# Kernel tuning notes

Measured on AMD Instinct MI355X. Metric: run time of the kernel, lower is better.

Reference implementation:

```python
import jax, jax.numpy as jnp
import numpy as np

B, H, W, C, D = 8, 64, 64, 128, 16


def setup_inputs() -> dict:
    key = jax.random.key(0)
    ks = jax.random.split(key, 6)
    scale = 1.0 / np.sqrt(C)
    return {
        "x": jax.random.normal(ks[0], (B, H, W, C), dtype=jnp.float32),
        "w_f": jax.random.normal(ks[1], (C, D), dtype=jnp.float32) * scale,
        "w_g": jax.random.normal(ks[2], (C, D), dtype=jnp.float32) * scale,
        "w_h": jax.random.normal(ks[3], (C, D), dtype=jnp.float32) * scale,
        "w_v": jax.random.normal(ks[4], (D, C), dtype=jnp.float32) * (1.0 / np.sqrt(D)),
        "gamma": jax.random.normal(ks[5], (1,), dtype=jnp.float32) * 0.1,
    }


def reference(x, w_f, w_g, w_h, w_v, gamma):
    b, h, w, c = x.shape
    n = h * w
    xf = x.reshape(b, n, c)                      # flatten spatial dims
    f = jnp.einsum('bnc,cd->bnd', xf, w_f)       # 1x1 conv == channel matmul
    g = jnp.einsum('bnc,cd->bnd', xf, w_g)
    hh = jnp.einsum('bnc,cd->bnd', xf, w_h)
    scores = jnp.einsum('bnd,bmd->bnm', f, g)    # [B, N, N], no 1/sqrt(d) scaling (faithful)
    attn = jax.nn.softmax(scores, axis=1)        # NOTE: softmax over axis=1 as in original
    y = jnp.einsum('bnm,bmd->bnd', attn, hh)     # [B, N, D]
    y = jnp.einsum('bnd,dc->bnc', y, w_v)        # output 1x1 conv
    y = y.reshape(b, h, w, c)
    return gamma * y + x
```

## Files before the change

### kernel.cpp

```cpp
#include <hip/hip_runtime.h>

typedef _Float16 f16;
typedef _Float16 f16x4 __attribute__((ext_vector_type(4)));
typedef _Float16 n16x2 __attribute__((ext_vector_type(2)));
typedef float    f32x4 __attribute__((ext_vector_type(4)));

#define LOG2E 1.44269504088896340736f
#define OFF25 36.0673760222824936f

__device__ __forceinline__ f32x4 MFMA(f16x4 a, f16x4 b, f32x4 c) {
#if defined(__HIP_DEVICE_COMPILE__)
    return __builtin_amdgcn_mfma_f32_16x16x16f16(a, b, c, 0, 0, 0);
#else
    return c;
#endif
}

__device__ __forceinline__ float fexp2(float x) {
#if defined(__HIP_DEVICE_COMPILE__)
    return __builtin_amdgcn_exp2f(x);
#else
    return exp2f(x);
#endif
}

__device__ __forceinline__ f16x4 pk4(float a, float b, float c, float d) {
#if defined(__HIP_DEVICE_COMPILE__)
    n16x2 lo = __builtin_bit_cast(n16x2, __builtin_amdgcn_cvt_pkrtz(a, b));
    n16x2 hi = __builtin_bit_cast(n16x2, __builtin_amdgcn_cvt_pkrtz(c, d));
    f16x4 r; r[0] = lo[0]; r[1] = lo[1]; r[2] = hi[0]; r[3] = hi[1];
    return r;
#else
    f16x4 r; r[0] = (f16)a; r[1] = (f16)b; r[2] = (f16)c; r[3] = (f16)d;
    return r;
#endif
}

__global__ __launch_bounds__(256) void k_proj(const float* __restrict__ x,
        const float* __restrict__ wf, const float* __restrict__ wg,
        const float* __restrict__ wh, f16* __restrict__ F,
        f16* __restrict__ G, float* __restrict__ Ht) {
    const int lane = threadIdx.x & 63;
    const int wid  = threadIdx.x >> 6;
    const int tile = wid >> 1;
    const int kh   = wid & 1;
    const int g16  = lane >> 4;
    const int c16  = lane & 15;
    const long r0  = ((long)blockIdx.x * 2 + tile) * 16;

    f16x4 bw[3][4];
    const float* Ws[3] = { wf, wg, wh };
    #pragma unroll
    for (int w = 0; w < 3; ++w)
        #pragma unroll
        for (int kk = 0; kk < 4; ++kk) {
            const int kb = (kh * 4 + kk) * 16 + g16 * 4;
            bw[w][kk] = pk4(Ws[w][(kb + 0) * 16 + c16], Ws[w][(kb + 1) * 16 + c16],
                            Ws[w][(kb + 2) * 16 + c16], Ws[w][(kb + 3) * 16 + c16]);
        }

    f32x4 af = {0,0,0,0}, ag = {0,0,0,0}, ah = {0,0,0,0};
    const float* xr = x + (r0 + c16) * 128;
    #pragma unroll
    for (int kk = 0; kk < 4; ++kk) {
        float4 xa = *(const float4*)(xr + (kh * 4 + kk) * 16 + g16 * 4);
        f16x4 a = pk4(xa.x, xa.y, xa.z, xa.w);
        af = MFMA(a, bw[0][kk], af);
        ag = MFMA(a, bw[1][kk], ag);
        ah = MFMA(a, bw[2][kk], ah);
    }

    __shared__ float red[2][64][13];
    if (kh == 1) {
        #pragma unroll
        for (int i = 0; i < 4; ++i) {
            red[tile][lane][i]     = af[i];
            red[tile][lane][4 + i] = ag[i];
            red[tile][lane][8 + i] = ah[i];
        }
    }
    __syncthreads();
    if (kh == 0) {
        #pragma unroll
        for (int i = 0; i < 4; ++i) {
            af[i] += red[tile][lane][i];
            ag[i] += red[tile][lane][4 + i];
            ah[i] += red[tile][lane][8 + i];
        }
        #pragma unroll
        for (int i = 0; i < 4; ++i) {
            const long row = r0 + g16 * 4 + i;
            F[row * 16 + c16] = (f16)(af[i] * LOG2E);
            G[row * 16 + c16] = (f16)ag[i];
        }
        float4 hv = make_float4(ah[0], ah[1], ah[2], ah[3]);
        *(float4*)(Ht + (long)c16 * 32768 + r0 + g16 * 4) = hv;
    }
}

__global__ __launch_bounds__(512) void k_cs(const f16* __restrict__ F,
        const f16* __restrict__ G, const float* __restrict__ Ht,
        float* __restrict__ nM2, f16* __restrict__ Hf) {
    const int lane = threadIdx.x & 63;
    const int tp   = threadIdx.x >> 6;
    const int b    = blockIdx.x >> 6;
    const int mb   = (blockIdx.x & 63) * 64;
    const int g16  = lane >> 4, c16 = lane & 15;
    const long bb  = (long)b * 4096;

    f16x4 ga[4];
    #pragma unroll
    for (int j = 0; j < 4; ++j)
        ga[j] = *(const f16x4*)(G + (bb + mb + 16 * j + c16) * 16 + g16 * 4);

    const f16* Fb = F + (bb + tp * 512) * 16;
    float qm[4][4], zs[4][4];
    #pragma unroll
    for (int j = 0; j < 4; ++j)
        #pragma unroll
        for (int i = 0; i < 4; ++i) { qm[j][i] = -1e30f; zs[j][i] = 0.f; }

    const f32x4 coff = {-OFF25, -OFF25, -OFF25, -OFF25};
    f16x4 fb0 = *(const f16x4*)(Fb + (c16) * 16 + g16 * 4);
    f16x4 fb1 = *(const f16x4*)(Fb + (16 + c16) * 16 + g16 * 4);
    f16x4 fb2 = *(const f16x4*)(Fb + (32 + c16) * 16 + g16 * 4);
    for (int t = 0; t < 32; ++t) {
        f16x4 fbn = *(const f16x4*)(Fb + ((t + 3) * 16 + c16) * 16 + g16 * 4);
        #pragma unroll
        for (int j = 0; j < 4; ++j) {
            f32x4 s = MFMA(ga[j], fb0, coff);
            #pragma unroll
            for (int i = 0; i < 4; ++i) {
                zs[j][i] += fexp2(s[i]);
                qm[j][i] = fmaxf(qm[j][i], s[i]);
            }
        }
        fb0 = fb1; fb1 = fb2; fb2 = fbn;
    }
    #pragma unroll
    for (int d = 8; d >= 1; d >>= 1)
        #pragma unroll
        for (int j = 0; j < 4; ++j)
            #pragma unroll
            for (int i = 0; i < 4; ++i) {
                qm[j][i] = fmaxf(qm[j][i], __shfl_xor(qm[j][i], d));
                zs[j][i] += __shfl_xor(zs[j][i], d);
            }

    __shared__ float lq[8][64], lz[8][64], lrz[64];
    if (c16 == 0) {
        #pragma unroll
        for (int j = 0; j < 4; ++j)
            #pragma unroll
            for (int i = 0; i < 4; ++i) {
                const int ml = 16 * j + 4 * g16 + i;
                lq[tp][ml] = qm[j][i];
                lz[tp][ml] = zs[j][i];
            }
    }
    __syncthreads();
    if (threadIdx.x < 64) {
        const int ml = threadIdx.x;
        float q = lq[0][ml], z = 0.f;
        #pragma unroll
        for (int p = 1; p < 8; ++p) q = fmaxf(q, lq[p][ml]);
        #pragma unroll
        for (int p = 0; p < 8; ++p) z += lz[p][ml];
        nM2[bb + mb + ml] = -q - OFF25;
        lrz[ml] = fexp2(q) / z;
    }
    __syncthreads();
    if (tp < 4) {
        const int ml0 = 16 * tp + 4 * g16;
        float4 hv = *(const float4*)(Ht + (long)c16 * 32768 + bb + mb + ml0);
        f32x4 rz = *(const f32x4*)&lrz[ml0];
        const long tileg = (bb + mb) / 16 + tp;
        *(f16x4*)(Hf + tileg * 256 + lane * 4) =
            pk4(hv.x * rz[0], hv.y * rz[1], hv.z * rz[2], hv.w * rz[3]);
    }
}

__global__ __launch_bounds__(512) void k_pv(const f16* __restrict__ F,
        const f16* __restrict__ G, const f16* __restrict__ Hf,
        const float* __restrict__ nM2, const float* __restrict__ wv,
        const float* __restrict__ xin, const float* __restrict__ gamma,
        float* __restrict__ out) {
    const int lane = threadIdx.x & 63;
    const int tp   = threadIdx.x >> 6;
    const int b    = blockIdx.x >> 6;
    const int n0   = (blockIdx.x & 63) * 64;
    const int g16  = lane >> 4, c16 = lane & 15;
    const long bb  = (long)b * 4096;

    f16x4 fbv[4];
    #pragma unroll
    for (int j = 0; j < 4; ++j)
        fbv[j] = *(const f16x4*)(F + (bb + n0 + 16 * j + c16) * 16 + g16 * 4);

    const int jo = tp >> 1, th = tp & 1;
    const float gm = gamma[0];
    f16x4 wvf[4];
    #pragma unroll
    for (int t = 0; t < 4; ++t) {
        const int c0 = (4 * th + t) * 16;
        wvf[t] = pk4(wv[(g16 * 4 + 0) * 128 + c0 + c16] * gm,
                     wv[(g16 * 4 + 1) * 128 + c0 + c16] * gm,
                     wv[(g16 * 4 + 2) * 128 + c0 + c16] * gm,
                     wv[(g16 * 4 + 3) * 128 + c0 + c16] * gm);
    }

    const f16* Gp = G + bb * 16;
    const f16* Hp = Hf + bb * 16 + lane * 4;
    const float* Np = nM2 + bb;
    const int mbase = tp * 512;

    f32x4 yT[4] = {{0,0,0,0},{0,0,0,0},{0,0,0,0},{0,0,0,0}};
    f16x4 ga0 = *(const f16x4*)(Gp + (mbase + c16) * 16 + g16 * 4);
    f16x4 ha0 = *(const f16x4*)(Hp + (long)mbase * 16);
    f32x4 nm0 = *(const f32x4*)(Np + mbase + g16 * 4);
    f16x4 ga1 = *(const f16x4*)(Gp + (mbase + 16 + c16) * 16 + g16 * 4);
    f16x4 ha1 = *(const f16x4*)(Hp + (long)(mbase + 16) * 16);
    f32x4 nm1 = *(const f32x4*)(Np + mbase + 16 + g16 * 4);
    f16x4 ga2 = *(const f16x4*)(Gp + (mbase + 32 + c16) * 16 + g16 * 4);
    f16x4 ha2 = *(const f16x4*)(Hp + (long)(mbase + 32) * 16);
    f32x4 nm2 = *(const f32x4*)(Np + mbase + 32 + g16 * 4);
    for (int t = 0; t < 32; ++t) {
        const int m3 = mbase + t * 16 + 48;
        f16x4 gan = *(const f16x4*)(Gp + (m3 + c16) * 16 + g16 * 4);
        f16x4 han = *(const f16x4*)(Hp + (long)m3 * 16);
        f32x4 nmn = *(const f32x4*)(Np + m3 + g16 * 4);
        #pragma unroll
        for (int j = 0; j < 4; ++j) {
            f32x4 s = MFMA(ga0, fbv[j], nm0);
            f16x4 pb = pk4(fexp2(s[0]), fexp2(s[1]),
                           fexp2(s[2]), fexp2(s[3]));
            yT[j] = MFMA(ha0, pb, yT[j]);
        }
        ga0 = ga1; ha0 = ha1; nm0 = nm1;
        ga1 = ga2; ha1 = ha2; nm1 = nm2;
        ga2 = gan; ha2 = han; nm2 = nmn;
    }

    __shared__ float red[8][4][64][5];
    #pragma unroll
    for (int j = 0; j < 4; ++j)
        #pragma unroll
        for (int i = 0; i < 4; ++i) red[tp][j][lane][i] = yT[j][i];
    __syncthreads();

    f32x4 ys = {0,0,0,0};
    #pragma unroll
    for (int p = 0; p < 8; ++p)
        #pragma unroll
        for (int i = 0; i < 4; ++i) ys[i] += red[p][jo][lane][i];
    const f16x4 ya = pk4(ys[0], ys[1], ys[2], ys[3]);

    #pragma unroll
    for (int t = 0; t < 4; ++t) {
        const int c0 = (4 * th + t) * 16;
        f32x4 zero = {0,0,0,0};
        f32x4 o = MFMA(ya, wvf[t], zero);
        #pragma unroll
        for (int i = 0; i < 4; ++i) {
            const long idx = (bb + n0 + 16 * jo + 4 * g16 + i) * 128 + c0 + c16;
            out[idx] = o[i] + xin[idx];
        }
    }
}

extern "C" void kernel_launch(void* const* d_in, const int* in_sizes, int n_in,
                              void* d_out, int out_size, void* d_ws, size_t ws_size,
                              hipStream_t stream) {
    const float* x     = (const float*)d_in[0];
    const float* wf    = (const float*)d_in[1];
    const float* wg    = (const float*)d_in[2];
    const float* wh    = (const float*)d_in[3];
    const float* wv    = (const float*)d_in[4];
    const float* gamma = (const float*)d_in[5];
    float* out = (float*)d_out;

    char* p = (char*)d_ws;
    const long BN  = 8L * 4096;
    const long PAD = 8192;
    f16*   F   = (f16*)p;    p += BN * 16 * sizeof(f16)   + PAD;
    f16*   G   = (f16*)p;    p += BN * 16 * sizeof(f16)   + PAD;
    float* Ht  = (float*)p;  p += 16 * BN * sizeof(float) + PAD;
    f16*   Hf  = (f16*)p;    p += 16 * BN * sizeof(f16)   + PAD;
    float* nM2 = (float*)p;  p += BN * sizeof(float)      + PAD;

    k_proj<<<1024, 256, 0, stream>>>(x, wf, wg, wh, F, G, Ht);
    k_cs  <<<512,  512, 0, stream>>>(F, G, Ht, nM2, Hf);
    k_pv  <<<512,  512, 0, stream>>>(F, G, Hf, nM2, wv, x, gamma, out);
}
```

Measured before the change: 54.44 us.

## Split attention reductions across two blocks with separate finalize and output kernels

Both the column-stats kernel and the PV kernel now split the reduction dimension in half across two blocks, doubling grid size from 512 to 1024 blocks so more CUs stay busy. Partial max/sum and partial Y results go to workspace, and two new kernels combine them: k_fin merges the stats and builds the scaled H, and k_out merges the Y halves and applies the Wv projection plus the gamma residual with scalar FMAs. This adds two extra launches and extra global traffic for the partials. It also moves the output projection off MFMA onto a plain per-element loop.

```diff
diff --git a/kernel.cpp b/kernel.cpp
--- a/kernel.cpp
+++ b/kernel.cpp
@@ -99,12 +99,14 @@
 }
 
 __global__ __launch_bounds__(512) void k_cs(const f16* __restrict__ F,
-        const f16* __restrict__ G, const float* __restrict__ Ht,
-        float* __restrict__ nM2, f16* __restrict__ Hf) {
+        const f16* __restrict__ G, float* __restrict__ QMp,
+        float* __restrict__ Zp) {
     const int lane = threadIdx.x & 63;
     const int tp   = threadIdx.x >> 6;
-    const int b    = blockIdx.x >> 6;
-    const int mb   = (blockIdx.x & 63) * 64;
+    const int bid  = blockIdx.x >> 1;
+    const int nh   = blockIdx.x & 1;
+    const int b    = bid >> 6;
+    const int mb   = (bid & 63) * 64;
     const int g16  = lane >> 4, c16 = lane & 15;
     const long bb  = (long)b * 4096;
 
@@ -113,7 +115,7 @@
     for (int j = 0; j < 4; ++j)
         ga[j] = *(const f16x4*)(G + (bb + mb + 16 * j + c16) * 16 + g16 * 4);
 
-    const f16* Fb = F + (bb + tp * 512) * 16;
+    const f16* Fb = F + (bb + nh * 2048 + tp * 256) * 16;
     float qm[4][4], zs[4][4];
     #pragma unroll
     for (int j = 0; j < 4; ++j)
@@ -124,7 +126,7 @@
     f16x4 fb0 = *(const f16x4*)(Fb + (c16) * 16 + g16 * 4);
     f16x4 fb1 = *(const f16x4*)(Fb + (16 + c16) * 16 + g16 * 4);
     f16x4 fb2 = *(const f16x4*)(Fb + (32 + c16) * 16 + g16 * 4);
-    for (int t = 0; t < 32; ++t) {
+    for (int t = 0; t < 16; ++t) {
         f16x4 fbn = *(const f16x4*)(Fb + ((t + 3) * 16 + c16) * 16 + g16 * 4);
         #pragma unroll
         for (int j = 0; j < 4; ++j) {
@@ -147,7 +149,7 @@
                 zs[j][i] += __shfl_xor(zs[j][i], d);
             }
 
-    __shared__ float lq[8][64], lz[8][64], lrz[64];
+    __shared__ float lq[8][64], lz[8][64];
     if (c16 == 0) {
         #pragma unroll
         for (int j = 0; j < 4; ++j)
@@ -166,29 +168,45 @@
         for (int p = 1; p < 8; ++p) q = fmaxf(q, lq[p][ml]);
         #pragma unroll
         for (int p = 0; p < 8; ++p) z += lz[p][ml];
-        nM2[bb + mb + ml] = -q - OFF25;
-        lrz[ml] = fexp2(q) / z;
-    }
-    __syncthreads();
-    if (tp < 4) {
-        const int ml0 = 16 * tp + 4 * g16;
-        float4 hv = *(const float4*)(Ht + (long)c16 * 32768 + bb + mb + ml0);
-        f32x4 rz = *(const f32x4*)&lrz[ml0];
-        const long tileg = (bb + mb) / 16 + tp;
-        *(f16x4*)(Hf + tileg * 256 + lane * 4) =
-            pk4(hv.x * rz[0], hv.y * rz[1], hv.z * rz[2], hv.w * rz[3]);
-    }
+        QMp[(long)nh * 32768 + bb + mb + ml] = q;
+        Zp [(long)nh * 32768 + bb + mb + ml] = z;
+    }
+}
+
+__global__ __launch_bounds__(256) void k_fin(const float* __restrict__ QMp,
+        const float* __restrict__ Zp, const float* __restrict__ Ht,
+        float* __restrict__ nM2, f16* __restrict__ Hf) {
+    const int lane = threadIdx.x & 63;
+    const int tp   = threadIdx.x >> 6;
+    const int g16  = lane >> 4, c16 = lane & 15;
+    const long m0  = (long)blockIdx.x * 64;
+
+    __shared__ float lrz[64];
+    if (threadIdx.x < 64) {
+        const long i = m0 + threadIdx.x;
+        const float q = fmaxf(QMp[i], QMp[32768 + i]);
+        const float z = Zp[i] + Zp[32768 + i];
+        nM2[i] = -q - OFF25;
+        lrz[threadIdx.x] = fexp2(q) / z;
+    }
+    __syncthreads();
+    const int ml0 = 16 * tp + 4 * g16;
+    float4 hv = *(const float4*)(Ht + (long)c16 * 32768 + m0 + ml0);
+    f32x4 rz = *(const f32x4*)&lrz[ml0];
+    const long tileg = m0 / 16 + tp;
+    *(f16x4*)(Hf + tileg * 256 + lane * 4) =
+        pk4(hv.x * rz[0], hv.y * rz[1], hv.z * rz[2], hv.w * rz[3]);
 }
 
 __global__ __launch_bounds__(512) void k_pv(const f16* __restrict__ F,
         const f16* __restrict__ G, const f16* __restrict__ Hf,
-        const float* __restrict__ nM2, const float* __restrict__ wv,
-        const float* __restrict__ xin, const float* __restrict__ gamma,
-        float* __restrict__ out) {
+        const float* __restrict__ nM2, float* __restrict__ Yp) {
     const int lane = threadIdx.x & 63;
     const int tp   = threadIdx.x >> 6;
-    const int b    = blockIdx.x >> 6;
-    const int n0   = (blockIdx.x & 63) * 64;
+    const int bid  = blockIdx.x >> 1;
+    const int mh   = blockIdx.x & 1;
+    const int b    = bid >> 6;
+    const int n0   = (bid & 63) * 64;
     const int g16  = lane >> 4, c16 = lane & 15;
     const long bb  = (long)b * 4096;
 
@@ -196,23 +214,11 @@
     #pragma unroll
     for (int j = 0; j < 4; ++j)
         fbv[j] = *(const f16x4*)(F + (bb + n0 + 16 * j + c16) * 16 + g16 * 4);
-
-    const int jo = tp >> 1, th = tp & 1;
-    const float gm = gamma[0];
-    f16x4 wvf[4];
-    #pragma unroll
-    for (int t = 0; t < 4; ++t) {
-        const int c0 = (4 * th + t) * 16;
-        wvf[t] = pk4(wv[(g16 * 4 + 0) * 128 + c0 + c16] * gm,
-                     wv[(g16 * 4 + 1) * 128 + c0 + c16] * gm,
-                     wv[(g16 * 4 + 2) * 128 + c0 + c16] * gm,
-                     wv[(g16 * 4 + 3) * 128 + c0 + c16] * gm);
-    }
 
     const f16* Gp = G + bb * 16;
     const f16* Hp = Hf + bb * 16 + lane * 4;
     const float* Np = nM2 + bb;
-    const int mbase = tp * 512;
+    const int mbase = mh * 2048 + tp * 256;
 
     f32x4 yT[4] = {{0,0,0,0},{0,0,0,0},{0,0,0,0},{0,0,0,0}};
     f16x4 ga0 = *(const f16x4*)(Gp + (mbase + c16) * 16 + g16 * 4);
@@ -224,7 +230,7 @@
     f16x4 ga2 = *(const f16x4*)(Gp + (mbase + 32 + c16) * 16 + g16 * 4);
     f16x4 ha2 = *(const f16x4*)(Hp + (long)(mbase + 32) * 16);
     f32x4 nm2 = *(const f32x4*)(Np + mbase + 32 + g16 * 4);
-    for (int t = 0; t < 32; ++t) {
+    for (int t = 0; t < 16; ++t) {
         const int m3 = mbase + t * 16 + 48;
         f16x4 gan = *(const f16x4*)(Gp + (m3 + c16) * 16 + g16 * 4);
         f16x4 han = *(const f16x4*)(Hp + (long)m3 * 16);
@@ -248,24 +254,35 @@
         for (int i = 0; i < 4; ++i) red[tp][j][lane][i] = yT[j][i];
     __syncthreads();
 
-    f32x4 ys = {0,0,0,0};
+    const int jo = tp >> 1, th = tp & 1;
+    float ys[2] = {0.f, 0.f};
     #pragma unroll
     for (int p = 0; p < 8; ++p)
         #pragma unroll
-        for (int i = 0; i < 4; ++i) ys[i] += red[p][jo][lane][i];
-    const f16x4 ya = pk4(ys[0], ys[1], ys[2], ys[3]);
-
-    #pragma unroll
-    for (int t = 0; t < 4; ++t) {
-        const int c0 = (4 * th + t) * 16;
-        f32x4 zero = {0,0,0,0};
-        f32x4 o = MFMA(ya, wvf[t], zero);
-        #pragma unroll
-        for (int i = 0; i < 4; ++i) {
-            const long idx = (bb + n0 + 16 * jo + 4 * g16 + i) * 128 + c0 + c16;
-            out[idx] = o[i] + xin[idx];
-        }
-    }
+        for (int k = 0; k < 2; ++k) ys[k] += red[p][jo][lane][2 * th + k];
+    float* yo = Yp + ((long)mh * 32768 + bb + n0 + 16 * jo + c16) * 16
+                   + 4 * g16 + 2 * th;
+    *(float2*)yo = make_float2(ys[0], ys[1]);
+}
+
+__global__ __launch_bounds__(256) void k_out(const float* __restrict__ Yp,
+        const float* __restrict__ wv, const float* __restrict__ xin,
+        const float* __restrict__ gamma, float* __restrict__ out) {
+    __shared__ float yl[2][16];
+    const long row0 = (long)blockIdx.x * 2;
+    if (threadIdx.x < 32) {
+        const int r = threadIdx.x >> 4, d = threadIdx.x & 15;
+        yl[r][d] = Yp[(row0 + r) * 16 + d] + Yp[32768L * 16 + (row0 + r) * 16 + d];
+    }
+    __syncthreads();
+    const long idx = (long)blockIdx.x * 256 + threadIdx.x;
+    const int  c = (int)(idx & 127);
+    const int  r = (threadIdx.x >> 7) & 1;
+    float s = 0.f;
+    #pragma unroll
+    for (int d = 0; d < 16; ++d)
+        s = fmaf(yl[r][d], wv[d * 128 + c], s);
+    out[idx] = fmaf(gamma[0], s, xin[idx]);
 }
 
 extern "C" void kernel_launch(void* const* d_in, const int* in_sizes, int n_in,
@@ -282,13 +299,18 @@
     char* p = (char*)d_ws;
     const long BN  = 8L * 4096;
     const long PAD = 8192;
-    f16*   F   = (f16*)p;    p += BN * 16 * sizeof(f16)   + PAD;
-    f16*   G   = (f16*)p;    p += BN * 16 * sizeof(f16)   + PAD;
-    float* Ht  = (float*)p;  p += 16 * BN * sizeof(float) + PAD;
-    f16*   Hf  = (f16*)p;    p += 16 * BN * sizeof(f16)   + PAD;
-    float* nM2 = (float*)p;  p += BN * sizeof(float)      + PAD;
-
-    k_proj<<<1024, 256, 0, stream>>>(x, wf, wg, wh, F, G, Ht);
-    k_cs  <<<512,  512, 0, stream>>>(F, G, Ht, nM2, Hf);
-    k_pv  <<<512,  512, 0, stream>>>(F, G, Hf, nM2, wv, x, gamma, out);
-}
+    f16*   F   = (f16*)p;    p += BN * 16 * sizeof(f16)      + PAD;
+    f16*   G   = (f16*)p;    p += BN * 16 * sizeof(f16)      + PAD;
+    float* Ht  = (float*)p;  p += 16 * BN * sizeof(float)    + PAD;
+    f16*   Hf  = (f16*)p;    p += 16 * BN * sizeof(f16)      + PAD;
+    float* nM2 = (float*)p;  p += BN * sizeof(float)         + PAD;
+    float* QMp = (float*)p;  p += 2 * BN * sizeof(float)     + PAD;
+    float* Zp  = (float*)p;  p += 2 * BN * sizeof(float)     + PAD;
+    float* Yp  = (float*)p;  p += 2 * BN * 16 * sizeof(float)+ PAD;
+
+    k_proj<<<1024,  256, 0, stream>>>(x, wf, wg, wh, F, G, Ht);
+    k_cs  <<<1024,  512, 0, stream>>>(F, G, QMp, Zp);
+    k_fin <<<512,   256, 0, stream>>>(QMp, Zp, Ht, nM2, Hf);
+    k_pv  <<<1024,  512, 0, stream>>>(F, G, Hf, nM2, Yp);
+    k_out <<<16384, 256, 0, stream>>>(Yp, wv, x, gamma, out);
+}
```

Result: slower. 74.85 us (+37.5%).

## Fold column-softmax normalizer into log-domain bias and write H directly as fp16

Applied to the files above, without the earlier changes.

The column-softmax normalizer is now carried entirely as a log2 bias, -log2(z) - OFF25, instead of being split into a running max and an exp2(max)/z factor applied to H. This removes the per-element max tracking and its shuffle and shared-memory reduction from k_cs, along with the second phase and barrier that rescaled H. k_proj writes H straight into the fp16 MFMA tile layout, so the fp32 transposed Ht buffer and its round trip through memory are gone. The risk is numerical: it relies on the fixed offset keeping exp2 sums in range, since there is no longer a max subtraction.

```diff
diff --git a/kernel.cpp b/kernel.cpp
--- a/kernel.cpp
+++ b/kernel.cpp
@@ -24,6 +24,14 @@
 #endif
 }
 
+__device__ __forceinline__ float flog2(float x) {
+#if defined(__HIP_DEVICE_COMPILE__)
+    return __builtin_amdgcn_logf(x);
+#else
+    return log2f(x);
+#endif
+}
+
 __device__ __forceinline__ f16x4 pk4(float a, float b, float c, float d) {
 #if defined(__HIP_DEVICE_COMPILE__)
     n16x2 lo = __builtin_bit_cast(n16x2, __builtin_amdgcn_cvt_pkrtz(a, b));
@@ -39,7 +47,7 @@
 __global__ __launch_bounds__(256) void k_proj(const float* __restrict__ x,
         const float* __restrict__ wf, const float* __restrict__ wg,
         const float* __restrict__ wh, f16* __restrict__ F,
-        f16* __restrict__ G, float* __restrict__ Ht) {
+        f16* __restrict__ G, f16* __restrict__ Hf) {
     const int lane = threadIdx.x & 63;
     const int wid  = threadIdx.x >> 6;
     const int tile = wid >> 1;
@@ -93,14 +101,13 @@
             F[row * 16 + c16] = (f16)(af[i] * LOG2E);
             G[row * 16 + c16] = (f16)ag[i];
         }
-        float4 hv = make_float4(ah[0], ah[1], ah[2], ah[3]);
-        *(float4*)(Ht + (long)c16 * 32768 + r0 + g16 * 4) = hv;
+        *(f16x4*)(Hf + (r0 >> 4) * 256 + lane * 4) =
+            pk4(ah[0], ah[1], ah[2], ah[3]);
     }
 }
 
 __global__ __launch_bounds__(512) void k_cs(const f16* __restrict__ F,
-        const f16* __restrict__ G, const float* __restrict__ Ht,
-        float* __restrict__ nM2, f16* __restrict__ Hf) {
+        const f16* __restrict__ G, float* __restrict__ nM2) {
     const int lane = threadIdx.x & 63;
     const int tp   = threadIdx.x >> 6;
     const int b    = blockIdx.x >> 6;
@@ -114,11 +121,11 @@
         ga[j] = *(const f16x4*)(G + (bb + mb + 16 * j + c16) * 16 + g16 * 4);
 
     const f16* Fb = F + (bb + tp * 512) * 16;
-    float qm[4][4], zs[4][4];
-    #pragma unroll
-    for (int j = 0; j < 4; ++j)
-        #pragma unroll
-        for (int i = 0; i < 4; ++i) { qm[j][i] = -1e30f; zs[j][i] = 0.f; }
+    float zs[4][4];
+    #pragma unroll
+    for (int j = 0; j < 4; ++j)
+        #pragma unroll
+        for (int i = 0; i < 4; ++i) zs[j][i] = 0.f;
 
     const f32x4 coff = {-OFF25, -OFF25, -OFF25, -OFF25};
     f16x4 fb0 = *(const f16x4*)(Fb + (c16) * 16 + g16 * 4);
@@ -130,10 +137,8 @@
         for (int j = 0; j < 4; ++j) {
             f32x4 s = MFMA(ga[j], fb0, coff);
             #pragma unroll
-            for (int i = 0; i < 4; ++i) {
+            for (int i = 0; i < 4; ++i)
                 zs[j][i] += fexp2(s[i]);
-                qm[j][i] = fmaxf(qm[j][i], s[i]);
-            }
         }
         fb0 = fb1; fb1 = fb2; fb2 = fbn;
     }
@@ -142,41 +147,24 @@
         #pragma unroll
         for (int j = 0; j < 4; ++j)
             #pragma unroll
-            for (int i = 0; i < 4; ++i) {
-                qm[j][i] = fmaxf(qm[j][i], __shfl_xor(qm[j][i], d));
+            for (int i = 0; i < 4; ++i)
                 zs[j][i] += __shfl_xor(zs[j][i], d);
-            }
-
-    __shared__ float lq[8][64], lz[8][64], lrz[64];
+
+    __shared__ float lz[8][64];
     if (c16 == 0) {
         #pragma unroll
         for (int j = 0; j < 4; ++j)
             #pragma unroll
-            for (int i = 0; i < 4; ++i) {
-                const int ml = 16 * j + 4 * g16 + i;
-                lq[tp][ml] = qm[j][i];
-                lz[tp][ml] = zs[j][i];
-            }
+            for (int i = 0; i < 4; ++i)
+                lz[tp][16 * j + 4 * g16 + i] = zs[j][i];
     }
     __syncthreads();
     if (threadIdx.x < 64) {
         const int ml = threadIdx.x;
-        float q = lq[0][ml], z = 0.f;
-        #pragma unroll
-        for (int p = 1; p < 8; ++p) q = fmaxf(q, lq[p][ml]);
+        float z = 0.f;
         #pragma unroll
         for (int p = 0; p < 8; ++p) z += lz[p][ml];
-        nM2[bb + mb + ml] = -q - OFF25;
-        lrz[ml] = fexp2(q) / z;
-    }
-    __syncthreads();
-    if (tp < 4) {
-        const int ml0 = 16 * tp + 4 * g16;
-        float4 hv = *(const float4*)(Ht + (long)c16 * 32768 + bb + mb + ml0);
-        f32x4 rz = *(const f32x4*)&lrz[ml0];
-        const long tileg = (bb + mb) / 16 + tp;
-        *(f16x4*)(Hf + tileg * 256 + lane * 4) =
-            pk4(hv.x * rz[0], hv.y * rz[1], hv.z * rz[2], hv.w * rz[3]);
+        nM2[bb + mb + ml] = -flog2(z) - OFF25;
     }
 }
 
@@ -282,13 +270,12 @@
     char* p = (char*)d_ws;
     const long BN  = 8L * 4096;
     const long PAD = 8192;
-    f16*   F   = (f16*)p;    p += BN * 16 * sizeof(f16)   + PAD;
-    f16*   G   = (f16*)p;    p += BN * 16 * sizeof(f16)   + PAD;
-    float* Ht  = (float*)p;  p += 16 * BN * sizeof(float) + PAD;
-    f16*   Hf  = (f16*)p;    p += 16 * BN * sizeof(f16)   + PAD;
-    float* nM2 = (float*)p;  p += BN * sizeof(float)      + PAD;
-
-    k_proj<<<1024, 256, 0, stream>>>(x, wf, wg, wh, F, G, Ht);
-    k_cs  <<<512,  512, 0, stream>>>(F, G, Ht, nM2, Hf);
+    f16*   F   = (f16*)p;    p += BN * 16 * sizeof(f16) + PAD;
+    f16*   G   = (f16*)p;    p += BN * 16 * sizeof(f16) + PAD;
+    f16*   Hf  = (f16*)p;    p += BN * 16 * sizeof(f16) + PAD;
+    float* nM2 = (float*)p;  p += BN * sizeof(float)    + PAD;
+
+    k_proj<<<1024, 256, 0, stream>>>(x, wf, wg, wh, F, G, Hf);
+    k_cs  <<<512,  512, 0, stream>>>(F, G, nM2);
     k_pv  <<<512,  512, 0, stream>>>(F, G, Hf, nM2, wv, x, gamma, out);
 }
```

After: 51.37 us. 5.6% less time.
